# Kernel tuning notes

Measured on AMD Instinct MI355X. Metric: run time of the kernel, lower is better.

The kernel has to match this reference:

```python
import jax, jax.numpy as jnp
import numpy as np

B = 4096      # batch (number of graphs / query nodes)
N = 524288    # total ball nodes (~128 per graph)
H = 128       # hidden_dim


def setup_inputs() -> dict:
    key = jax.random.key(0)
    ks = jax.random.split(key, 12)
    s = 0.05
    return {
        "query": jax.random.normal(ks[0], (B, H), dtype=jnp.float32),
        "ball": jax.random.normal(ks[1], (N, H), dtype=jnp.float32),
        "ball_batch": jnp.sort(jax.random.randint(ks[2], (N,), 0, B, dtype=jnp.int32)),
        # ball_attention: Linear(H, H//2) -> Tanh -> Linear(H//2, 1)
        "attn_w1": jax.random.normal(ks[3], (H, H // 2), dtype=jnp.float32) * s,
        "attn_b1": jnp.zeros((H // 2,), dtype=jnp.float32),
        "attn_w2": jax.random.normal(ks[4], (H // 2, 1), dtype=jnp.float32) * s,
        "attn_b2": jnp.zeros((1,), dtype=jnp.float32),
        # combiner: Linear(2H, H) -> LayerNorm(H) -> GELU
        "comb_w": jax.random.normal(ks[5], (2 * H, H), dtype=jnp.float32) * s,
        "comb_b": jnp.zeros((H,), dtype=jnp.float32),
        "ln_g": jnp.ones((H,), dtype=jnp.float32),
        "ln_b": jnp.zeros((H,), dtype=jnp.float32),
        # boundary head: Linear(H, H//2) -> ReLU -> Linear(H//2, 1)
        "bnd_w1": jax.random.normal(ks[6], (H, H // 2), dtype=jnp.float32) * s,
        "bnd_b1": jnp.zeros((H // 2,), dtype=jnp.float32),
        "bnd_w2": jax.random.normal(ks[7], (H // 2, 1), dtype=jnp.float32) * s,
        "bnd_b2": jnp.zeros((1,), dtype=jnp.float32),
        # wicket head: Linear(H, H//2) -> ReLU -> Linear(H//2, 1)
        "wkt_w1": jax.random.normal(ks[8], (H, H // 2), dtype=jnp.float32) * s,
        "wkt_b1": jnp.zeros((H // 2,), dtype=jnp.float32),
        "wkt_w2": jax.random.normal(ks[9], (H // 2, 1), dtype=jnp.float32) * s,
        "wkt_b2": jnp.zeros((1,), dtype=jnp.float32),
    }


def reference(query, ball, ball_batch, attn_w1, attn_b1, attn_w2, attn_b2,
              comb_w, comb_b, ln_g, ln_b,
              bnd_w1, bnd_b1, bnd_w2, bnd_b2,
              wkt_w1, wkt_b1, wkt_w2, wkt_b2):
    nb = query.shape[0]  # static batch size
    # attention score MLP over ball nodes -> [N]
    scores = (jnp.tanh(ball @ attn_w1 + attn_b1) @ attn_w2 + attn_b2)[:, 0]
    # segment softmax (stable: subtract per-segment max)
    seg_max = jax.ops.segment_max(scores, ball_batch, num_segments=nb)
    e = jnp.exp(scores - seg_max[ball_batch])
    denom = jax.ops.segment_sum(e, ball_batch, num_segments=nb)
    w = e / denom[ball_batch]
    # weighted-sum pooling -> [B, H]
    pooled = jax.ops.segment_sum(w[:, None] * ball, ball_batch, num_segments=nb)
    # concat + combiner: Linear -> LayerNorm -> GELU (exact, torch default)
    h = jnp.concatenate([query, pooled], axis=-1) @ comb_w + comb_b
    mu = jnp.mean(h, axis=-1, keepdims=True)
    var = jnp.mean((h - mu) ** 2, axis=-1, keepdims=True)
    h = (h - mu) / jnp.sqrt(var + 1e-5) * ln_g + ln_b
    h = jax.nn.gelu(h, approximate=False)
    boundary = jax.nn.relu(h @ bnd_w1 + bnd_b1) @ bnd_w2 + bnd_b2
    wicket = jax.nn.relu(h @ wkt_w1 + wkt_b1) @ wkt_w2 + wkt_b2
    return boundary, wicket
```

## Files before the change

### kernel.cpp

```cpp
#include <hip/hip_runtime.h>
#include <math.h>

#define N_NODES 524288
#define BATCH   4096
#define HID     128

typedef __attribute__((ext_vector_type(8))) short bf16x8;
typedef __attribute__((ext_vector_type(4))) float f32x4;

__device__ __forceinline__ unsigned short f2bf(float f) {
  unsigned int u = __float_as_uint(f);
  u = (u + 0x7FFFu + ((u >> 16) & 1u)) >> 16;
  return (unsigned short)u;
}

__global__ __launch_bounds__(256) void k_scores(
    const float* __restrict__ ball, const float* __restrict__ w1,
    const float* __restrict__ b1, const float* __restrict__ w2,
    const float* __restrict__ b2, float* __restrict__ scores, int nTiles)
{
  const int lane = threadIdx.x & 63;
  const int m16  = lane & 15;
  const int quad = lane >> 4;
  const int gwave  = blockIdx.x * 4 + (threadIdx.x >> 6);
  const int nWaves = gridDim.x * 4;

  bf16x8 fb[4][4];
  for (int t = 0; t < 4; ++t) {
    const int n = t * 16 + m16;
    for (int s = 0; s < 4; ++s) {
      const int k0 = s * 32 + quad * 8;
      bf16x8 v;
      #pragma unroll
      for (int j = 0; j < 8; ++j) v[j] = (short)f2bf(w1[(k0 + j) * 64 + n]);
      fb[t][s] = v;
    }
  }
  float b1v[4], w2v[4];
  #pragma unroll
  for (int t = 0; t < 4; ++t) { b1v[t] = b1[t*16 + m16]; w2v[t] = w2[t*16 + m16]; }
  const float b2v = b2[0];

  for (int tile = gwave; tile < nTiles; tile += nWaves) {
    const float* rowp = ball + ((size_t)(tile * 16 + m16)) * HID + quad * 8;
    f32x4 acc0 = {0.f,0.f,0.f,0.f}, acc1 = {0.f,0.f,0.f,0.f};
    f32x4 acc2 = {0.f,0.f,0.f,0.f}, acc3 = {0.f,0.f,0.f,0.f};
    #pragma unroll
    for (int s = 0; s < 4; ++s) {
      const float4* p = (const float4*)(rowp + s * 32);
      float4 x0 = p[0], x1 = p[1];
      bf16x8 fa;
      fa[0]=(short)f2bf(x0.x); fa[1]=(short)f2bf(x0.y);
      fa[2]=(short)f2bf(x0.z); fa[3]=(short)f2bf(x0.w);
      fa[4]=(short)f2bf(x1.x); fa[5]=(short)f2bf(x1.y);
      fa[6]=(short)f2bf(x1.z); fa[7]=(short)f2bf(x1.w);
      acc0 = __builtin_amdgcn_mfma_f32_16x16x32_bf16(fa, fb[0][s], acc0, 0,0,0);
      acc1 = __builtin_amdgcn_mfma_f32_16x16x32_bf16(fa, fb[1][s], acc1, 0,0,0);
      acc2 = __builtin_amdgcn_mfma_f32_16x16x32_bf16(fa, fb[2][s], acc2, 0,0,0);
      acc3 = __builtin_amdgcn_mfma_f32_16x16x32_bf16(fa, fb[3][s], acc3, 0,0,0);
    }
    #pragma unroll
    for (int r = 0; r < 4; ++r) {
      float p = tanhf(acc0[r] + b1v[0]) * w2v[0]
              + tanhf(acc1[r] + b1v[1]) * w2v[1]
              + tanhf(acc2[r] + b1v[2]) * w2v[2]
              + tanhf(acc3[r] + b1v[3]) * w2v[3];
      p += __shfl_xor(p, 1); p += __shfl_xor(p, 2);
      p += __shfl_xor(p, 4); p += __shfl_xor(p, 8);
      if (m16 == 0) scores[tile * 16 + quad * 4 + r] = p + b2v;
    }
  }
}

__global__ __launch_bounds__(64) void k_pool(
    const float* __restrict__ ball, const int* __restrict__ bb,
    const float* __restrict__ scores, float* __restrict__ pooled, int N)
{
  const int b = blockIdx.x;
  const int lane = threadIdx.x;

  int lo = 0, hi = N;
  while (lo < hi) { int mid = (lo + hi) >> 1; if (bb[mid] < b) lo = mid + 1; else hi = mid; }
  const int start = lo;
  hi = N;
  while (lo < hi) { int mid = (lo + hi) >> 1; if (bb[mid] < b + 1) lo = mid + 1; else hi = mid; }
  const int end = lo;

  float2* out = (float2*)(pooled + (size_t)b * HID);
  if (start >= end) { out[lane] = make_float2(0.f, 0.f); return; }

  float m = -INFINITY;
  for (int i = start + lane; i < end; i += 64) m = fmaxf(m, scores[i]);
  #pragma unroll
  for (int o = 32; o; o >>= 1) m = fmaxf(m, __shfl_xor(m, o));

  float d = 0.f;
  for (int i = start + lane; i < end; i += 64) d += expf(scores[i] - m);
  #pragma unroll
  for (int o = 32; o; o >>= 1) d += __shfl_xor(d, o);
  const float inv = 1.f / d;

  float2 acc = make_float2(0.f, 0.f);
  int i = start;
  for (; i + 3 < end; i += 4) {
    float w0 = expf(scores[i+0] - m) * inv;
    float w1 = expf(scores[i+1] - m) * inv;
    float w2 = expf(scores[i+2] - m) * inv;
    float w3 = expf(scores[i+3] - m) * inv;
    float2 v0 = ((const float2*)(ball + (size_t)(i+0) * HID))[lane];
    float2 v1 = ((const float2*)(ball + (size_t)(i+1) * HID))[lane];
    float2 v2 = ((const float2*)(ball + (size_t)(i+2) * HID))[lane];
    float2 v3 = ((const float2*)(ball + (size_t)(i+3) * HID))[lane];
    acc.x += w0*v0.x + w1*v1.x + w2*v2.x + w3*v3.x;
    acc.y += w0*v0.y + w1*v1.y + w2*v2.y + w3*v3.y;
  }
  for (; i < end; ++i) {
    float w = expf(scores[i] - m) * inv;
    float2 v = ((const float2*)(ball + (size_t)i * HID))[lane];
    acc.x += w*v.x; acc.y += w*v.y;
  }
  out[lane] = acc;
}

__global__ __launch_bounds__(128) void k_combine(
    const float* __restrict__ query, const float* __restrict__ pooled,
    const float* __restrict__ cw, const float* __restrict__ cb,
    const float* __restrict__ lg, const float* __restrict__ lb,
    const float* __restrict__ bw1, const float* __restrict__ bb1,
    const float* __restrict__ bw2, const float* __restrict__ bb2,
    const float* __restrict__ ww1, const float* __restrict__ wb1,
    const float* __restrict__ ww2, const float* __restrict__ wb2,
    float* __restrict__ out)
{
  __shared__ float in_lds[256][8];
  __shared__ float h_lds[128][8];
  __shared__ float part[2][2][8];
  const int tid  = threadIdx.x;
  const int row0 = blockIdx.x * 8;

  for (int idx = tid; idx < 2048; idx += 128) {
    const int k = idx >> 3, r = idx & 7;
    float v = (k < 128) ? query[(size_t)(row0 + r) * 128 + k]
                        : pooled[(size_t)(row0 + r) * 128 + (k - 128)];
    in_lds[k][r] = v;
  }
  __syncthreads();

  const int j = tid;
  float acc[8];
  const float cbj = cb[j];
  #pragma unroll
  for (int r = 0; r < 8; ++r) acc[r] = cbj;
  for (int k = 0; k < 256; ++k) {
    const float w = cw[k * 128 + j];
    #pragma unroll
    for (int r = 0; r < 8; ++r) acc[r] = fmaf(in_lds[k][r], w, acc[r]);
  }

  const int wv = tid >> 6, ln = tid & 63;
  #pragma unroll
  for (int r = 0; r < 8; ++r) {
    float v = acc[r], v2 = v * v;
    #pragma unroll
    for (int o = 32; o; o >>= 1) { v += __shfl_xor(v, o); v2 += __shfl_xor(v2, o); }
    if (ln == 0) { part[0][wv][r] = v; part[1][wv][r] = v2; }
  }
  __syncthreads();
  const float gj = lg[j], bj = lb[j];
  #pragma unroll
  for (int r = 0; r < 8; ++r) {
    const float S = part[0][0][r] + part[0][1][r];
    const float Q = part[1][0][r] + part[1][1][r];
    const float mean = S * (1.f / 128.f);
    const float var  = Q * (1.f / 128.f) - mean * mean;
    const float rs   = rsqrtf(var + 1e-5f);
    float x = (acc[r] - mean) * rs * gj + bj;
    x = 0.5f * x * (1.f + erff(x * 0.70710678118654752f));
    h_lds[j][r] = x;
  }
  __syncthreads();

  const float* W1 = wv ? ww1 : bw1;
  const float* B1 = wv ? wb1 : bb1;
  const float* W2 = wv ? ww2 : bw2;
  const float  B2 = wv ? wb2[0] : bb2[0];
  float t[8];
  const float b1l = B1[ln];
  #pragma unroll
  for (int r = 0; r < 8; ++r) t[r] = b1l;
  for (int k = 0; k < 128; ++k) {
    const float w = W1[k * 64 + ln];
    #pragma unroll
    for (int r = 0; r < 8; ++r) t[r] = fmaf(h_lds[k][r], w, t[r]);
  }
  const float w2l = W2[ln];
  #pragma unroll
  for (int r = 0; r < 8; ++r) {
    float o = fmaxf(t[r], 0.f) * w2l;
    #pragma unroll
    for (int m = 32; m; m >>= 1) o += __shfl_xor(o, m);
    if (ln == 0) out[wv * BATCH + row0 + r] = o + B2;
  }
}

extern "C" void kernel_launch(void* const* d_in, const int* in_sizes, int n_in,
                              void* d_out, int out_size, void* d_ws, size_t ws_size,
                              hipStream_t stream)
{
  const float* query = (const float*)d_in[0];
  const float* ball  = (const float*)d_in[1];
  const int*   bb    = (const int*)  d_in[2];
  const float* aw1   = (const float*)d_in[3];
  const float* ab1   = (const float*)d_in[4];
  const float* aw2   = (const float*)d_in[5];
  const float* ab2   = (const float*)d_in[6];
  const float* cw    = (const float*)d_in[7];
  const float* cb    = (const float*)d_in[8];
  const float* lg    = (const float*)d_in[9];
  const float* lbeta = (const float*)d_in[10];
  const float* bw1   = (const float*)d_in[11];
  const float* bb1   = (const float*)d_in[12];
  const float* bw2   = (const float*)d_in[13];
  const float* bb2   = (const float*)d_in[14];
  const float* ww1   = (const float*)d_in[15];
  const float* wb1   = (const float*)d_in[16];
  const float* ww2   = (const float*)d_in[17];
  const float* wb2   = (const float*)d_in[18];

  float* scores = (float*)d_ws;
  float* pooled = scores + N_NODES;
  float* out    = (float*)d_out;

  k_scores<<<1024, 256, 0, stream>>>(ball, aw1, ab1, aw2, ab2, scores, N_NODES / 16);
  k_pool<<<BATCH, 64, 0, stream>>>(ball, bb, scores, pooled, N_NODES);
  k_combine<<<BATCH / 8, 128, 0, stream>>>(query, pooled, cw, cb, lg, lbeta,
                                           bw1, bb1, bw2, bb2, ww1, wb1, ww2, wb2, out);
}
```

Before: 489.2 us.

## Fuse attention scoring into per-segment pooling kernel with LDS score buffer

```diff
diff --git a/kernel.cpp b/kernel.cpp
--- a/kernel.cpp
+++ b/kernel.cpp
@@ -4,6 +4,7 @@
 #define N_NODES 524288
 #define BATCH   4096
 #define HID     128
+#define MAXL    1024
 
 typedef __attribute__((ext_vector_type(8))) short bf16x8;
 typedef __attribute__((ext_vector_type(4))) float f32x4;
@@ -14,16 +15,29 @@
   return (unsigned short)u;
 }
 
-__global__ __launch_bounds__(256) void k_scores(
-    const float* __restrict__ ball, const float* __restrict__ w1,
-    const float* __restrict__ b1, const float* __restrict__ w2,
-    const float* __restrict__ b2, float* __restrict__ scores, int nTiles)
+__global__ __launch_bounds__(64) void k_score_pool(
+    const float* __restrict__ ball, const int* __restrict__ bb,
+    const float* __restrict__ w1, const float* __restrict__ b1,
+    const float* __restrict__ w2, const float* __restrict__ b2,
+    float* __restrict__ pooled, int N)
 {
-  const int lane = threadIdx.x & 63;
+  __shared__ float s_e[MAXL];
+  const int lane = threadIdx.x;
   const int m16  = lane & 15;
   const int quad = lane >> 4;
-  const int gwave  = blockIdx.x * 4 + (threadIdx.x >> 6);
-  const int nWaves = gridDim.x * 4;
+  const int b    = blockIdx.x;
+
+  int lo = 0, hi = N;
+  while (lo < hi) { int mid = (lo + hi) >> 1; if (bb[mid] < b) lo = mid + 1; else hi = mid; }
+  const int start = lo;
+  hi = N;
+  while (lo < hi) { int mid = (lo + hi) >> 1; if (bb[mid] < b + 1) lo = mid + 1; else hi = mid; }
+  const int end = lo;
+  int L = end - start;
+
+  float4* outp = (float4*)(pooled + (size_t)b * HID);
+  if (L <= 0) { if (lane < 32) outp[lane] = make_float4(0.f, 0.f, 0.f, 0.f); return; }
+  if (L > MAXL) L = MAXL;
 
   bf16x8 fb[4][4];
   for (int t = 0; t < 4; ++t) {
@@ -41,8 +55,10 @@
   for (int t = 0; t < 4; ++t) { b1v[t] = b1[t*16 + m16]; w2v[t] = w2[t*16 + m16]; }
   const float b2v = b2[0];
 
-  for (int tile = gwave; tile < nTiles; tile += nWaves) {
-    const float* rowp = ball + ((size_t)(tile * 16 + m16)) * HID + quad * 8;
+  for (int t0 = 0; t0 < L; t0 += 16) {
+    int row = start + t0 + m16;
+    if (row > N - 1) row = N - 1;
+    const float* rowp = ball + (size_t)row * HID + quad * 8;
     f32x4 acc0 = {0.f,0.f,0.f,0.f}, acc1 = {0.f,0.f,0.f,0.f};
     f32x4 acc2 = {0.f,0.f,0.f,0.f}, acc3 = {0.f,0.f,0.f,0.f};
     #pragma unroll
@@ -67,59 +83,66 @@
               + tanhf(acc3[r] + b1v[3]) * w2v[3];
       p += __shfl_xor(p, 1); p += __shfl_xor(p, 2);
       p += __shfl_xor(p, 4); p += __shfl_xor(p, 8);
-      if (m16 == 0) scores[tile * 16 + quad * 4 + r] = p + b2v;
-    }
-  }
-}
-
-__global__ __launch_bounds__(64) void k_pool(
-    const float* __restrict__ ball, const int* __restrict__ bb,
-    const float* __restrict__ scores, float* __restrict__ pooled, int N)
-{
-  const int b = blockIdx.x;
-  const int lane = threadIdx.x;
-
-  int lo = 0, hi = N;
-  while (lo < hi) { int mid = (lo + hi) >> 1; if (bb[mid] < b) lo = mid + 1; else hi = mid; }
-  const int start = lo;
-  hi = N;
-  while (lo < hi) { int mid = (lo + hi) >> 1; if (bb[mid] < b + 1) lo = mid + 1; else hi = mid; }
-  const int end = lo;
-
-  float2* out = (float2*)(pooled + (size_t)b * HID);
-  if (start >= end) { out[lane] = make_float2(0.f, 0.f); return; }
+      const int idx = t0 + quad * 4 + r;
+      if (m16 == 0 && idx < L) s_e[idx] = p + b2v;
+    }
+  }
+  __syncthreads();
 
   float m = -INFINITY;
-  for (int i = start + lane; i < end; i += 64) m = fmaxf(m, scores[i]);
+  for (int i = lane; i < L; i += 64) m = fmaxf(m, s_e[i]);
   #pragma unroll
   for (int o = 32; o; o >>= 1) m = fmaxf(m, __shfl_xor(m, o));
 
   float d = 0.f;
-  for (int i = start + lane; i < end; i += 64) d += expf(scores[i] - m);
+  for (int i = lane; i < L; i += 64) { float e = expf(s_e[i] - m); s_e[i] = e; d += e; }
+  __syncthreads();
   #pragma unroll
   for (int o = 32; o; o >>= 1) d += __shfl_xor(d, o);
   const float inv = 1.f / d;
 
-  float2 acc = make_float2(0.f, 0.f);
+  const int lh = lane >> 5;
+  const int c4 = lane & 31;
+  float4 acc = {0.f, 0.f, 0.f, 0.f};
   int i = start;
-  for (; i + 3 < end; i += 4) {
-    float w0 = expf(scores[i+0] - m) * inv;
-    float w1 = expf(scores[i+1] - m) * inv;
-    float w2 = expf(scores[i+2] - m) * inv;
-    float w3 = expf(scores[i+3] - m) * inv;
-    float2 v0 = ((const float2*)(ball + (size_t)(i+0) * HID))[lane];
-    float2 v1 = ((const float2*)(ball + (size_t)(i+1) * HID))[lane];
-    float2 v2 = ((const float2*)(ball + (size_t)(i+2) * HID))[lane];
-    float2 v3 = ((const float2*)(ball + (size_t)(i+3) * HID))[lane];
-    acc.x += w0*v0.x + w1*v1.x + w2*v2.x + w3*v3.x;
-    acc.y += w0*v0.y + w1*v1.y + w2*v2.y + w3*v3.y;
-  }
-  for (; i < end; ++i) {
-    float w = expf(scores[i] - m) * inv;
-    float2 v = ((const float2*)(ball + (size_t)i * HID))[lane];
-    acc.x += w*v.x; acc.y += w*v.y;
-  }
-  out[lane] = acc;
+  for (; i + 8 <= end; i += 8) {
+    #pragma unroll
+    for (int u = 0; u < 4; ++u) {
+      const int row = i + 2 * u + lh;
+      const float w = s_e[row - start];
+      const float4 v = ((const float4*)(ball + (size_t)row * HID))[c4];
+      acc.x = fmaf(w, v.x, acc.x);
+      acc.y = fmaf(w, v.y, acc.y);
+      acc.z = fmaf(w, v.z, acc.z);
+      acc.w = fmaf(w, v.w, acc.w);
+    }
+  }
+  for (; i + 2 <= end; i += 2) {
+    const int row = i + lh;
+    const float w = s_e[row - start];
+    const float4 v = ((const float4*)(ball + (size_t)row * HID))[c4];
+    acc.x = fmaf(w, v.x, acc.x);
+    acc.y = fmaf(w, v.y, acc.y);
+    acc.z = fmaf(w, v.z, acc.z);
+    acc.w = fmaf(w, v.w, acc.w);
+  }
+  if (i < end && lh == 0) {
+    const int row = i;
+    const float w = s_e[row - start];
+    const float4 v = ((const float4*)(ball + (size_t)row * HID))[c4];
+    acc.x = fmaf(w, v.x, acc.x);
+    acc.y = fmaf(w, v.y, acc.y);
+    acc.z = fmaf(w, v.z, acc.z);
+    acc.w = fmaf(w, v.w, acc.w);
+  }
+  acc.x += __shfl_xor(acc.x, 32);
+  acc.y += __shfl_xor(acc.y, 32);
+  acc.z += __shfl_xor(acc.z, 32);
+  acc.w += __shfl_xor(acc.w, 32);
+  if (lh == 0) {
+    acc.x *= inv; acc.y *= inv; acc.z *= inv; acc.w *= inv;
+    outp[c4] = acc;
+  }
 }
 
 __global__ __launch_bounds__(128) void k_combine(
@@ -227,12 +250,10 @@
   const float* ww2   = (const float*)d_in[17];
   const float* wb2   = (const float*)d_in[18];
 
-  float* scores = (float*)d_ws;
-  float* pooled = scores + N_NODES;
+  float* pooled = (float*)d_ws;
   float* out    = (float*)d_out;
 
-  k_scores<<<1024, 256, 0, stream>>>(ball, aw1, ab1, aw2, ab2, scores, N_NODES / 16);
-  k_pool<<<BATCH, 64, 0, stream>>>(ball, bb, scores, pooled, N_NODES);
+  k_score_pool<<<BATCH, 64, 0, stream>>>(ball, bb, aw1, ab1, aw2, ab2, pooled, N_NODES);
   k_combine<<<BATCH / 8, 128, 0, stream>>>(query, pooled, cw, cb, lg, lbeta,
                                            bw1, bb1, bw2, bb2, ww1, wb1, ww2, wb2, out);
 }
```

After: 482.4 us. About the same (-1.4%).
